# Kernel tuning notes

Hardware: AMD Instinct MI355X
Metric: run time of the kernel (lower is better)

## Reference

```python
import jax, jax.numpy as jnp
import numpy as np

NUM_AGENTS = 1000
N_ACTIONS = 16
HIDDEN = 256
COMM_STEPS = 4
B, M = 1024, 64


def setup_inputs() -> dict:
    key = jax.random.key(0)
    ks = jax.random.split(key, 8)
    agent_ids = jax.random.randint(ks[0], (B, M), 0, NUM_AGENTS)
    emb = jax.random.normal(ks[1], (NUM_AGENTS, HIDDEN), dtype=jnp.float32) * 0.1
    s1 = 1.0 / np.sqrt(3 * HIDDEN)
    W1 = jax.random.uniform(ks[2], (3 * HIDDEN, HIDDEN), jnp.float32, -s1, s1)
    b1 = jax.random.uniform(ks[3], (HIDDEN,), jnp.float32, -s1, s1)
    s2 = 1.0 / np.sqrt(HIDDEN)
    W2 = jax.random.uniform(ks[4], (HIDDEN, HIDDEN), jnp.float32, -s2, s2)
    b2 = jax.random.uniform(ks[5], (HIDDEN,), jnp.float32, -s2, s2)
    Wd = jax.random.uniform(ks[6], (HIDDEN, N_ACTIONS), jnp.float32, -s2, s2)
    bd = jax.random.uniform(ks[7], (N_ACTIONS,), jnp.float32, -s2, s2)
    return {"agent_ids": agent_ids, "emb": emb, "W1": W1, "b1": b1,
            "W2": W2, "b2": b2, "Wd": Wd, "bd": bd}


def reference(agent_ids, emb, W1, b1, W2, b2, Wd, bd):
    # h0: (B, M, H) embedding lookup
    h0 = emb[agent_ids]
    h = h0
    m = agent_ids.shape[1]
    inv = 1.0 / (m - 1)
    for _ in range(COMM_STEPS):
        # mean of other agents' hidden states: c_j = (sum_k h_k - h_j)/(M-1)
        c = (jnp.sum(h, axis=1, keepdims=True) - h) * inv
        x = jnp.concatenate([h, c, h0], axis=-1)  # (B, M, 3H)
        delta = jax.nn.relu(jnp.einsum('bmi,ih->bmh', x, W1) + b1)
        delta = jnp.einsum('bmi,ih->bmh', delta, W2) + b2
        h = h + delta  # residual (use_skip=True)
    logits = jnp.einsum('bmh,ha->bma', h, Wd) + bd
    return logits
```

## Files before the change

kernel.cpp:

```cpp
#include <hip/hip_runtime.h>

#define HID 256
#define NB 1024
#define NACT 16
#define HSTRIDE 528

typedef __bf16 bf16x8 __attribute__((ext_vector_type(8)));
typedef float  f32x4  __attribute__((ext_vector_type(4)));

#define HA_LO   33792
#define S_OFF   67584
#define LDS_TOT 68608

#define PREP_N (4 * 65536 + 4096)

__device__ __forceinline__ unsigned short f2bf(float x) {
    union { __bf16 b; unsigned short u; } v; v.b = (__bf16)x; return v.u;
}
__device__ __forceinline__ float bf2f(unsigned short u) {
    union { unsigned short u; __bf16 b; } v; v.u = u; return (float)v.b;
}
__device__ __forceinline__ float b2f_lo(unsigned v) { return bf2f((unsigned short)(v & 0xffffu)); }
__device__ __forceinline__ float b2f_hi(unsigned v) { return bf2f((unsigned short)(v >> 16)); }
__device__ __forceinline__ unsigned pack2(float a, float b) {
    return (unsigned)f2bf(a) | ((unsigned)f2bf(b) << 16);
}

__global__ __launch_bounds__(256) void prep_k(const float* __restrict__ W1,
                                              const float* __restrict__ W2,
                                              const float* __restrict__ Wd,
                                              unsigned short* __restrict__ WAh, unsigned short* __restrict__ WAl,
                                              unsigned short* __restrict__ WHh, unsigned short* __restrict__ WHl,
                                              unsigned short* __restrict__ WBh, unsigned short* __restrict__ WBl,
                                              unsigned short* __restrict__ WCh, unsigned short* __restrict__ WCl,
                                              unsigned short* __restrict__ WDh, unsigned short* __restrict__ WDl) {
    int i = blockIdx.x * 256 + threadIdx.x;
    const float inv = 1.0f / 63.0f;
    if (i < 4 * 65536) {
        int mat = i >> 16, j = i & 65535;
        int kq = j >> 13, r = j & 8191;
        int nb = r >> 9, r2 = r & 511;
        int l = r2 >> 3, e = r2 & 7;
        int n = nb * 16 + (l & 15);
        int k = kq * 32 + (l >> 4) * 8 + e;
        float val;
        if (mat == 0)      val = W1[k * 256 + n] - inv * W1[(256 + k) * 256 + n];
        else if (mat == 1) val = W1[(512 + k) * 256 + n];
        else if (mat == 2) val = W2[k * 256 + n];
        else               val = inv * W1[(256 + k) * 256 + n];
        unsigned short hi = f2bf(val);
        unsigned short lo = f2bf(val - bf2f(hi));
        if (mat == 0)      { WAh[j] = hi; WAl[j] = lo; }
        else if (mat == 1) { WHh[j] = hi; WHl[j] = lo; }
        else if (mat == 2) { WBh[j] = hi; WBl[j] = lo; }
        else               { WCh[j] = hi; WCl[j] = lo; }
    } else if (i < PREP_N) {
        int j = i - 4 * 65536, a = j >> 8, k = j & 255;
        float val = Wd[k * 16 + a];
        unsigned short hi = f2bf(val);
        WDh[j] = hi; WDl[j] = f2bf(val - bf2f(hi));
    }
}

__device__ __forceinline__ void kloopL2(const unsigned short* __restrict__ Wfh,
                                        const unsigned short* __restrict__ Wfl,
                                        const char* hA, f32x4 (&acc)[4][2],
                                        size_t lbase, int l15, int g)
{
    #pragma unroll 2
    for (int kq = 0; kq < 8; ++kq) {
        const int cb = kq * 64 + g * 16;
        bf16x8 ah[4], al[4];
        #pragma unroll
        for (int mt = 0; mt < 4; ++mt) {
            int rb = (mt * 16 + l15) * HSTRIDE;
            ah[mt] = *(const bf16x8*)(hA + rb + cb);
            al[mt] = *(const bf16x8*)(hA + HA_LO + rb + cb);
        }
        const size_t kb = (size_t)kq * 8192 + lbase;
        #pragma unroll
        for (int nt = 0; nt < 2; ++nt) {
            bf16x8 bh = *(const bf16x8*)(Wfh + kb + nt * 512);
            bf16x8 bl = *(const bf16x8*)(Wfl + kb + nt * 512);
            #pragma unroll
            for (int mt = 0; mt < 4; ++mt) {
                acc[mt][nt] = __builtin_amdgcn_mfma_f32_16x16x32_bf16(bh, ah[mt], acc[mt][nt], 0, 0, 0);
                acc[mt][nt] = __builtin_amdgcn_mfma_f32_16x16x32_bf16(bh, al[mt], acc[mt][nt], 0, 0, 0);
                acc[mt][nt] = __builtin_amdgcn_mfma_f32_16x16x32_bf16(bl, ah[mt], acc[mt][nt], 0, 0, 0);
            }
        }
    }
}

__global__ __launch_bounds__(512, 2) void fused_all(
    const int* __restrict__ ids, const float* __restrict__ emb,
    const unsigned short* __restrict__ WAh, const unsigned short* __restrict__ WAl,
    const unsigned short* __restrict__ WHh, const unsigned short* __restrict__ WHl,
    const unsigned short* __restrict__ WBh, const unsigned short* __restrict__ WBl,
    const unsigned short* __restrict__ WCh, const unsigned short* __restrict__ WCl,
    const unsigned short* __restrict__ WDh, const unsigned short* __restrict__ WDl,
    const float* __restrict__ b1, const float* __restrict__ b2,
    const float* __restrict__ bd, float* __restrict__ out)
{
    __shared__ __align__(16) char lds[LDS_TOT];
    const int tid = threadIdx.x;
    const int lane = tid & 63;
    const int w = tid >> 6;
    const int l15 = lane & 15, g = lane >> 4;
    const size_t rowbase = (size_t)blockIdx.x * 64;
    char* hA = lds;
    float* Sf = (float*)(lds + S_OFF);
    const size_t lbase = ((size_t)(w * 2) * 64 + lane) * 8;
    const int cb0 = w * 32 + g * 4;

    {
        int r = tid >> 3, c0 = (tid & 7) * 32;
        const float4* src = (const float4*)(emb + (size_t)ids[rowbase + r] * HID + c0);
        char* dh = hA + r * HSTRIDE + c0 * 2;
        #pragma unroll
        for (int j = 0; j < 8; ++j) {
            float4 v = src[j];
            unsigned short h0 = f2bf(v.x), h1 = f2bf(v.y), h2 = f2bf(v.z), h3 = f2bf(v.w);
            unsigned short q0 = f2bf(v.x - bf2f(h0)), q1 = f2bf(v.y - bf2f(h1)),
                           q2 = f2bf(v.z - bf2f(h2)), q3 = f2bf(v.w - bf2f(h3));
            *(uint2*)(dh + j * 8) = make_uint2((unsigned)h0 | ((unsigned)h1 << 16),
                                               (unsigned)h2 | ((unsigned)h3 << 16));
            *(uint2*)(dh + HA_LO + j * 8) = make_uint2((unsigned)q0 | ((unsigned)q1 << 16),
                                                       (unsigned)q2 | ((unsigned)q3 << 16));
        }
    }
    __syncthreads();

    if (tid < 256) {
        float ssum = 0.f;
        #pragma unroll 8
        for (int m = 0; m < 64; ++m) {
            int byte = m * HSTRIDE + tid * 2;
            ssum += bf2f(*(const unsigned short*)(hA + byte))
                  + bf2f(*(const unsigned short*)(hA + HA_LO + byte));
        }
        Sf[tid] = ssum;
    }
    __syncthreads();

    f32x4 acc[4][2], u0r[4][2];
    #pragma unroll
    for (int mt = 0; mt < 4; ++mt)
        #pragma unroll
        for (int nt = 0; nt < 2; ++nt) acc[mt][nt] = (f32x4){0.f, 0.f, 0.f, 0.f};

    kloopL2(WHh, WHl, hA, acc, lbase, l15, g);
    #pragma unroll
    for (int nt = 0; nt < 2; ++nt) {
        f32x4 b1v = *(const f32x4*)(b1 + cb0 + nt * 16);
        #pragma unroll
        for (int mt = 0; mt < 4; ++mt)
            u0r[mt][nt] = acc[mt][nt] + b1v;
    }

    for (int s = 0; s < 4; ++s) {
        f32x4 tacc[2];
        tacc[0] = tacc[1] = (f32x4){0.f, 0.f, 0.f, 0.f};
        #pragma unroll 2
        for (int kq = 0; kq < 8; ++kq) {
            const float* sp = Sf + kq * 32 + g * 8;
            f32x4 sa = *(const f32x4*)sp;
            f32x4 sb = *(const f32x4*)(sp + 4);
            bf16x8 shv, slv;
            #pragma unroll
            for (int e = 0; e < 8; ++e) {
                float sv = (e < 4) ? sa[e] : sb[e - 4];
                unsigned short h = f2bf(sv);
                ((unsigned short*)&shv)[e] = h;
                ((unsigned short*)&slv)[e] = f2bf(sv - bf2f(h));
            }
            const size_t kb = (size_t)kq * 8192 + lbase;
            #pragma unroll
            for (int nt = 0; nt < 2; ++nt) {
                bf16x8 wch = *(const bf16x8*)(WCh + kb + nt * 512);
                bf16x8 wcl = *(const bf16x8*)(WCl + kb + nt * 512);
                tacc[nt] = __builtin_amdgcn_mfma_f32_16x16x32_bf16(wch, shv, tacc[nt], 0, 0, 0);
                tacc[nt] = __builtin_amdgcn_mfma_f32_16x16x32_bf16(wch, slv, tacc[nt], 0, 0, 0);
                tacc[nt] = __builtin_amdgcn_mfma_f32_16x16x32_bf16(wcl, shv, tacc[nt], 0, 0, 0);
            }
        }

        #pragma unroll
        for (int mt = 0; mt < 4; ++mt)
            #pragma unroll
            for (int nt = 0; nt < 2; ++nt)
                acc[mt][nt] = u0r[mt][nt] + tacc[nt];
        kloopL2(WAh, WAl, hA, acc, lbase, l15, g);

        __syncthreads();
        {
            f32x4 b2v0 = *(const f32x4*)(b2 + cb0);
            f32x4 b2v1 = *(const f32x4*)(b2 + cb0 + 16);
            #pragma unroll
            for (int mt = 0; mt < 4; ++mt)
                #pragma unroll
                for (int nt = 0; nt < 2; ++nt) {
                    int byte = (mt * 16 + l15) * HSTRIDE + (cb0 + nt * 16) * 2;
                    uint2 ph = *(const uint2*)(hA + byte);
                    uint2 pl = *(const uint2*)(hA + HA_LO + byte);
                    f32x4 hres;
                    hres[0] = b2f_lo(ph.x) + b2f_lo(pl.x);
                    hres[1] = b2f_hi(ph.x) + b2f_hi(pl.x);
                    hres[2] = b2f_lo(ph.y) + b2f_lo(pl.y);
                    hres[3] = b2f_hi(ph.y) + b2f_hi(pl.y);
                    f32x4 av = acc[mt][nt];
                    float a0 = fmaxf(av[0], 0.f), a1 = fmaxf(av[1], 0.f);
                    float a2 = fmaxf(av[2], 0.f), a3 = fmaxf(av[3], 0.f);
                    unsigned h01 = pack2(a0, a1), h23 = pack2(a2, a3);
                    float r0 = a0 - bf2f((unsigned short)h01);
                    float r1 = a1 - bf2f((unsigned short)(h01 >> 16));
                    float r2 = a2 - bf2f((unsigned short)h23);
                    float r3 = a3 - bf2f((unsigned short)(h23 >> 16));
                    *(uint2*)(hA + byte) = make_uint2(h01, h23);
                    *(uint2*)(hA + HA_LO + byte) = make_uint2(pack2(r0, r1), pack2(r2, r3));
                    acc[mt][nt] = hres + (nt ? b2v1 : b2v0);
                }
        }
        __syncthreads();

        kloopL2(WBh, WBl, hA, acc, lbase, l15, g);

        __syncthreads();
        #pragma unroll
        for (int mt = 0; mt < 4; ++mt)
            #pragma unroll
            for (int nt = 0; nt < 2; ++nt) {
                int byte = (mt * 16 + l15) * HSTRIDE + (cb0 + nt * 16) * 2;
                f32x4 av = acc[mt][nt];
                unsigned h01 = pack2(av[0], av[1]), h23 = pack2(av[2], av[3]);
                float r0 = av[0] - bf2f((unsigned short)h01);
                float r1 = av[1] - bf2f((unsigned short)(h01 >> 16));
                float r2 = av[2] - bf2f((unsigned short)h23);
                float r3 = av[3] - bf2f((unsigned short)(h23 >> 16));
                *(uint2*)(hA + byte) = make_uint2(h01, h23);
                *(uint2*)(hA + HA_LO + byte) = make_uint2(pack2(r0, r1), pack2(r2, r3));
            }
        if (s < 3) {
            #pragma unroll
            for (int nt = 0; nt < 2; ++nt) {
                f32x4 cs = (acc[0][nt] + acc[1][nt]) + (acc[2][nt] + acc[3][nt]);
                #pragma unroll
                for (int d = 1; d < 16; d <<= 1) {
                    cs[0] += __shfl_xor(cs[0], d);
                    cs[1] += __shfl_xor(cs[1], d);
                    cs[2] += __shfl_xor(cs[2], d);
                    cs[3] += __shfl_xor(cs[3], d);
                }
                if (l15 == 0) *(f32x4*)(Sf + cb0 + nt * 16) = cs;
            }
        }
        __syncthreads();
    }

    if (w < 4) {
        f32x4 dacc = (f32x4){0.f, 0.f, 0.f, 0.f};
        #pragma unroll 2
        for (int kq = 0; kq < 8; ++kq) {
            int byte = (w * 16 + l15) * HSTRIDE + kq * 64 + g * 16;
            bf16x8 hh = *(const bf16x8*)(hA + byte);
            bf16x8 hl = *(const bf16x8*)(hA + HA_LO + byte);
            const int k = kq * 32;
            bf16x8 wdh = *(const bf16x8*)(WDh + (size_t)l15 * 256 + k + g * 8);
            bf16x8 wdl = *(const bf16x8*)(WDl + (size_t)l15 * 256 + k + g * 8);
            dacc = __builtin_amdgcn_mfma_f32_16x16x32_bf16(wdh, hh, dacc, 0, 0, 0);
            dacc = __builtin_amdgcn_mfma_f32_16x16x32_bf16(wdh, hl, dacc, 0, 0, 0);
            dacc = __builtin_amdgcn_mfma_f32_16x16x32_bf16(wdl, hh, dacc, 0, 0, 0);
        }
        f32x4 bdv = *(const f32x4*)(bd + g * 4);
        f32x4 o = dacc + bdv;
        *(f32x4*)(out + (rowbase + w * 16 + l15) * NACT + g * 4) = o;
    }
}

extern "C" void kernel_launch(void* const* d_in, const int* in_sizes, int n_in,
                              void* d_out, int out_size, void* d_ws, size_t ws_size,
                              hipStream_t stream) {
    const int*   ids = (const int*)d_in[0];
    const float* emb = (const float*)d_in[1];
    const float* W1  = (const float*)d_in[2];
    const float* b1  = (const float*)d_in[3];
    const float* W2  = (const float*)d_in[4];
    const float* b2  = (const float*)d_in[5];
    const float* Wd  = (const float*)d_in[6];
    const float* bd  = (const float*)d_in[7];
    float* out = (float*)d_out;

    char* p = (char*)d_ws;
    unsigned short* WAh = (unsigned short*)p; p += 65536 * 2;
    unsigned short* WAl = (unsigned short*)p; p += 65536 * 2;
    unsigned short* WHh = (unsigned short*)p; p += 65536 * 2;
    unsigned short* WHl = (unsigned short*)p; p += 65536 * 2;
    unsigned short* WBh = (unsigned short*)p; p += 65536 * 2;
    unsigned short* WBl = (unsigned short*)p; p += 65536 * 2;
    unsigned short* WCh = (unsigned short*)p; p += 65536 * 2;
    unsigned short* WCl = (unsigned short*)p; p += 65536 * 2;
    unsigned short* WDh = (unsigned short*)p; p += 4096 * 2;
    unsigned short* WDl = (unsigned short*)p; p += 4096 * 2;

    prep_k<<<(PREP_N + 255) / 256, 256, 0, stream>>>(W1, W2, Wd, WAh, WAl, WHh, WHl,
                                                     WBh, WBl, WCh, WCl, WDh, WDl);
    fused_all<<<NB, 512, 0, stream>>>(ids, emb, WAh, WAl, WHh, WHl, WBh, WBl,
                                      WCh, WCl, WDh, WDl, b1, b2, bd, out);
}
```

Before: 266.2 us.

## Permute LDS column layout of hidden state to cut bank conflicts

```diff
diff --git a/kernel.cpp b/kernel.cpp
--- a/kernel.cpp
+++ b/kernel.cpp
@@ -69,7 +69,7 @@
 {
     #pragma unroll 2
     for (int kq = 0; kq < 8; ++kq) {
-        const int cb = kq * 64 + g * 16;
+        const int cb = g * 128 + kq * 16;
         bf16x8 ah[4], al[4];
         #pragma unroll
         for (int mt = 0; mt < 4; ++mt) {
@@ -113,29 +113,38 @@
     const size_t lbase = ((size_t)(w * 2) * 64 + lane) * 8;
     const int cb0 = w * 32 + g * 4;
 
+    int colb[2];
+    #pragma unroll
+    for (int nt = 0; nt < 2; ++nt) {
+        int o = w * 4 + nt * 2 + (g >> 1);
+        colb[nt] = ((o & 3) * 8 + (o >> 2)) * 16 + (g & 1) * 8;
+    }
+
     {
-        int r = tid >> 3, c0 = (tid & 7) * 32;
-        const float4* src = (const float4*)(emb + (size_t)ids[rowbase + r] * HID + c0);
-        char* dh = hA + r * HSTRIDE + c0 * 2;
+        int r = tid >> 3, c0q = tid & 7;
+        const float4* src = (const float4*)(emb + (size_t)ids[rowbase + r] * HID + c0q * 32);
+        char* dh = hA + r * HSTRIDE;
         #pragma unroll
         for (int j = 0; j < 8; ++j) {
             float4 v = src[j];
             unsigned short h0 = f2bf(v.x), h1 = f2bf(v.y), h2 = f2bf(v.z), h3 = f2bf(v.w);
             unsigned short q0 = f2bf(v.x - bf2f(h0)), q1 = f2bf(v.y - bf2f(h1)),
                            q2 = f2bf(v.z - bf2f(h2)), q3 = f2bf(v.w - bf2f(h3));
-            *(uint2*)(dh + j * 8) = make_uint2((unsigned)h0 | ((unsigned)h1 << 16),
-                                               (unsigned)h2 | ((unsigned)h3 << 16));
-            *(uint2*)(dh + HA_LO + j * 8) = make_uint2((unsigned)q0 | ((unsigned)q1 << 16),
-                                                       (unsigned)q2 | ((unsigned)q3 << 16));
+            int byte = (j >> 1) * 128 + c0q * 16 + (j & 1) * 8;
+            *(uint2*)(dh + byte) = make_uint2((unsigned)h0 | ((unsigned)h1 << 16),
+                                              (unsigned)h2 | ((unsigned)h3 << 16));
+            *(uint2*)(dh + HA_LO + byte) = make_uint2((unsigned)q0 | ((unsigned)q1 << 16),
+                                                      (unsigned)q2 | ((unsigned)q3 << 16));
         }
     }
     __syncthreads();
 
     if (tid < 256) {
+        int cperm = (((tid >> 3) & 3) * 8 + (tid >> 5)) * 16 + (tid & 7) * 2;
         float ssum = 0.f;
         #pragma unroll 8
         for (int m = 0; m < 64; ++m) {
-            int byte = m * HSTRIDE + tid * 2;
+            int byte = m * HSTRIDE + cperm;
             ssum += bf2f(*(const unsigned short*)(hA + byte))
                   + bf2f(*(const unsigned short*)(hA + HA_LO + byte));
         }
@@ -166,14 +175,15 @@
             const float* sp = Sf + kq * 32 + g * 8;
             f32x4 sa = *(const f32x4*)sp;
             f32x4 sb = *(const f32x4*)(sp + 4);
-            bf16x8 shv, slv;
-            #pragma unroll
-            for (int e = 0; e < 8; ++e) {
-                float sv = (e < 4) ? sa[e] : sb[e - 4];
-                unsigned short h = f2bf(sv);
-                ((unsigned short*)&shv)[e] = h;
-                ((unsigned short*)&slv)[e] = f2bf(sv - bf2f(h));
-            }
+            unsigned sh[4], sl[4];
+            sh[0] = pack2(sa[0], sa[1]); sh[1] = pack2(sa[2], sa[3]);
+            sh[2] = pack2(sb[0], sb[1]); sh[3] = pack2(sb[2], sb[3]);
+            sl[0] = pack2(sa[0] - b2f_lo(sh[0]), sa[1] - b2f_hi(sh[0]));
+            sl[1] = pack2(sa[2] - b2f_lo(sh[1]), sa[3] - b2f_hi(sh[1]));
+            sl[2] = pack2(sb[0] - b2f_lo(sh[2]), sb[1] - b2f_hi(sh[2]));
+            sl[3] = pack2(sb[2] - b2f_lo(sh[3]), sb[3] - b2f_hi(sh[3]));
+            bf16x8 shv = *(const bf16x8*)sh;
+            bf16x8 slv = *(const bf16x8*)sl;
             const size_t kb = (size_t)kq * 8192 + lbase;
             #pragma unroll
             for (int nt = 0; nt < 2; ++nt) {
@@ -193,34 +203,31 @@
         kloopL2(WAh, WAl, hA, acc, lbase, l15, g);
 
         __syncthreads();
-        {
-            f32x4 b2v0 = *(const f32x4*)(b2 + cb0);
-            f32x4 b2v1 = *(const f32x4*)(b2 + cb0 + 16);
-            #pragma unroll
-            for (int mt = 0; mt < 4; ++mt)
-                #pragma unroll
-                for (int nt = 0; nt < 2; ++nt) {
-                    int byte = (mt * 16 + l15) * HSTRIDE + (cb0 + nt * 16) * 2;
-                    uint2 ph = *(const uint2*)(hA + byte);
-                    uint2 pl = *(const uint2*)(hA + HA_LO + byte);
-                    f32x4 hres;
-                    hres[0] = b2f_lo(ph.x) + b2f_lo(pl.x);
-                    hres[1] = b2f_hi(ph.x) + b2f_hi(pl.x);
-                    hres[2] = b2f_lo(ph.y) + b2f_lo(pl.y);
-                    hres[3] = b2f_hi(ph.y) + b2f_hi(pl.y);
-                    f32x4 av = acc[mt][nt];
-                    float a0 = fmaxf(av[0], 0.f), a1 = fmaxf(av[1], 0.f);
-                    float a2 = fmaxf(av[2], 0.f), a3 = fmaxf(av[3], 0.f);
-                    unsigned h01 = pack2(a0, a1), h23 = pack2(a2, a3);
-                    float r0 = a0 - bf2f((unsigned short)h01);
-                    float r1 = a1 - bf2f((unsigned short)(h01 >> 16));
-                    float r2 = a2 - bf2f((unsigned short)h23);
-                    float r3 = a3 - bf2f((unsigned short)(h23 >> 16));
-                    *(uint2*)(hA + byte) = make_uint2(h01, h23);
-                    *(uint2*)(hA + HA_LO + byte) = make_uint2(pack2(r0, r1), pack2(r2, r3));
-                    acc[mt][nt] = hres + (nt ? b2v1 : b2v0);
-                }
-        }
+        #pragma unroll
+        for (int mt = 0; mt < 4; ++mt)
+            #pragma unroll
+            for (int nt = 0; nt < 2; ++nt) {
+                f32x4 b2v = *(const f32x4*)(b2 + cb0 + nt * 16);
+                int byte = (mt * 16 + l15) * HSTRIDE + colb[nt];
+                uint2 ph = *(const uint2*)(hA + byte);
+                uint2 pl = *(const uint2*)(hA + HA_LO + byte);
+                f32x4 hres;
+                hres[0] = b2f_lo(ph.x) + b2f_lo(pl.x);
+                hres[1] = b2f_hi(ph.x) + b2f_hi(pl.x);
+                hres[2] = b2f_lo(ph.y) + b2f_lo(pl.y);
+                hres[3] = b2f_hi(ph.y) + b2f_hi(pl.y);
+                f32x4 av = acc[mt][nt];
+                float a0 = fmaxf(av[0], 0.f), a1 = fmaxf(av[1], 0.f);
+                float a2 = fmaxf(av[2], 0.f), a3 = fmaxf(av[3], 0.f);
+                unsigned h01 = pack2(a0, a1), h23 = pack2(a2, a3);
+                float r0 = a0 - b2f_lo(h01);
+                float r1 = a1 - b2f_hi(h01);
+                float r2 = a2 - b2f_lo(h23);
+                float r3 = a3 - b2f_hi(h23);
+                *(uint2*)(hA + byte) = make_uint2(h01, h23);
+                *(uint2*)(hA + HA_LO + byte) = make_uint2(pack2(r0, r1), pack2(r2, r3));
+                acc[mt][nt] = hres + b2v;
+            }
         __syncthreads();
 
         kloopL2(WBh, WBl, hA, acc, lbase, l15, g);
@@ -230,13 +237,13 @@
         for (int mt = 0; mt < 4; ++mt)
             #pragma unroll
             for (int nt = 0; nt < 2; ++nt) {
-                int byte = (mt * 16 + l15) * HSTRIDE + (cb0 + nt * 16) * 2;
+                int byte = (mt * 16 + l15) * HSTRIDE + colb[nt];
                 f32x4 av = acc[mt][nt];
                 unsigned h01 = pack2(av[0], av[1]), h23 = pack2(av[2], av[3]);
-                float r0 = av[0] - bf2f((unsigned short)h01);
-                float r1 = av[1] - bf2f((unsigned short)(h01 >> 16));
-                float r2 = av[2] - bf2f((unsigned short)h23);
-                float r3 = av[3] - bf2f((unsigned short)(h23 >> 16));
+                float r0 = av[0] - b2f_lo(h01);
+                float r1 = av[1] - b2f_hi(h01);
+                float r2 = av[2] - b2f_lo(h23);
+                float r3 = av[3] - b2f_hi(h23);
                 *(uint2*)(hA + byte) = make_uint2(h01, h23);
                 *(uint2*)(hA + HA_LO + byte) = make_uint2(pack2(r0, r1), pack2(r2, r3));
             }
@@ -261,7 +268,7 @@
         f32x4 dacc = (f32x4){0.f, 0.f, 0.f, 0.f};
         #pragma unroll 2
         for (int kq = 0; kq < 8; ++kq) {
-            int byte = (w * 16 + l15) * HSTRIDE + kq * 64 + g * 16;
+            int byte = (w * 16 + l15) * HSTRIDE + g * 128 + kq * 16;
             bf16x8 hh = *(const bf16x8*)(hA + byte);
             bf16x8 hl = *(const bf16x8*)(hA + HA_LO + byte);
             const int k = kq * 32;
```

Result: slower. 278.4 us (+4.6%).
